# Kernel tuning notes

Measured on AMD Instinct MI355X. Metric: run time of the kernel, lower is better.

Reference implementation:

```python
import jax, jax.numpy as jnp
import numpy as np
from jax import lax

COEF = 0.97  # rnn.weight_hh_l0; weight_ih_l0 == 1.0


def setup_inputs() -> dict:
    key = jax.random.key(0)
    B, C, T = 128, 1, 262144
    x = jax.random.normal(key, (B, C, T), dtype=jnp.float32)
    return {"input": x}


def reference(input) -> jnp.ndarray:
    # torch.nn.RNN(1,1,1,bias=False) with weight_ih=1, weight_hh=COEF and
    # default nonlinearity='tanh':  h[t] = tanh(x[t] + COEF * h[t-1])
    x = input[:, 0, :]                     # [B, T]
    B = x.shape[0]

    def step(h, x_t):                      # h: [B], x_t: [B]
        h = jnp.tanh(x_t + COEF * h)
        return h, h

    h0 = jnp.zeros((B,), dtype=x.dtype)
    _, ys = lax.scan(step, h0, x.T)        # ys: [T, B]
    return ys.T[:, None, :]                # [B, 1, T]
```

## Files before the change

### kernel.cpp

```cpp
#include <hip/hip_runtime.h>


#define BB 128
#define TT 262144
#define LL 128
#define WW 64
#define KK 32
#define RR ((WW + LL) / KK)
#define WR (WW / KK)

typedef float f32x4 __attribute__((ext_vector_type(4)));

__global__ __launch_bounds__(256) void ipe_kernel(const float* __restrict__ x,
                                                  float* __restrict__ y) {
    const int tid  = threadIdx.x;
    const int lane = tid & 63;
    const int wv   = tid >> 6;
    const int w    = blockIdx.x * 4 + wv;
    const int wavesPerRow = (TT / LL) / 64;
    const int row  = w / wavesPerRow;
    const int qg   = w % wavesPerRow;
    const int s0   = qg * 64;
    const size_t rowBase = (size_t)row * TT;

    __shared__ float tile_all[4][64][36];
    float (*tile)[36] = tile_all[wv];

    const int ls = lane & 7;
    const int le = lane >> 3;
    const long loadBase = (long)(s0 + ls) * LL - WW + 4 * le;

    f32x4 pfA[8], pfB[8];

    auto issue = [&](f32x4 (&pf)[8], int r) {
        #pragma unroll
        for (int m = 0; m < 8; ++m) {
            const long t = loadBase + (long)m * 8 * LL + (long)r * KK;
            if (t >= 0) pf[m] = *reinterpret_cast<const f32x4*>(x + rowBase + t);
            else        pf[m] = (f32x4){0.f, 0.f, 0.f, 0.f};
        }
    };

    const float C2 = 2.885390081777926815f;
    const float K2 = 0.97f * C2;
    float h = 0.f;

    issue(pfA, 0);

    auto round = [&](f32x4 (&cur)[8], f32x4 (&nxt)[8], int r) {
        if (r + 1 < RR) issue(nxt, r + 1);

        #pragma unroll
        for (int m = 0; m < 8; ++m)
            *reinterpret_cast<f32x4*>(&tile[8 * m + ls][4 * le]) = cur[m];
        asm volatile("" ::: "memory");

        float xv[KK];
        #pragma unroll
        for (int e = 0; e < 8; ++e) {
            f32x4 v = *reinterpret_cast<const f32x4*>(&tile[lane][4 * e]);
            xv[4 * e + 0] = v.x; xv[4 * e + 1] = v.y;
            xv[4 * e + 2] = v.z; xv[4 * e + 3] = v.w;
        }

        #pragma unroll
        for (int k = 0; k < KK; ++k) {
            float z2 = fmaf(K2, h, xv[k] * C2);
            float ez = __builtin_amdgcn_exp2f(z2);
            float rc = __builtin_amdgcn_rcpf(ez + 1.0f);
            h = fmaf(-2.0f, rc, 1.0f);
            xv[k] = h;
        }

        if (r >= WR) {
            asm volatile("" ::: "memory");
            #pragma unroll
            for (int e = 0; e < 8; ++e) {
                f32x4 v;
                v.x = xv[4 * e + 0]; v.y = xv[4 * e + 1];
                v.z = xv[4 * e + 2]; v.w = xv[4 * e + 3];
                *reinterpret_cast<f32x4*>(&tile[lane][4 * e]) = v;
            }
            asm volatile("" ::: "memory");
            #pragma unroll
            for (int m = 0; m < 8; ++m) {
                f32x4 v = *reinterpret_cast<const f32x4*>(&tile[8 * m + ls][4 * le]);
                const long t = loadBase + (long)m * 8 * LL + (long)r * KK;
                __builtin_nontemporal_store(v, reinterpret_cast<f32x4*>(y + rowBase + t));
            }
        }
        asm volatile("" ::: "memory");
    };

    #pragma unroll 1
    for (int r = 0; r < RR; r += 2) {
        round(pfA, pfB, r);
        round(pfB, pfA, r + 1);
    }
}

extern "C" void kernel_launch(void* const* d_in, const int* in_sizes, int n_in,
                              void* d_out, int out_size, void* d_ws, size_t ws_size,
                              hipStream_t stream) {
    const float* x = (const float*)d_in[0];
    float* y = (float*)d_out;
    const int blocks = (BB * (TT / LL)) / (4 * 64);
    ipe_kernel<<<dim3(blocks), dim3(256), 0, stream>>>(x, y);
}
```

Measured before the change: 56.75 us.

## Use single-wave blocks with 64-step chunks, one-shot load, and swizzled LDS

Each 64-lane block now handles 64 consecutive chunks of 64 timesteps. It loads the whole span plus a 64-element warm-up window in one shot, replacing the double-buffered 32-step rounds of 128-step segments. The LDS tile uses an XOR swizzle instead of padding to avoid bank conflicts. Block IDs are remapped across XCDs, and the stores change from nontemporal to regular. The warm-up-to-output ratio rises from 1:2 to 1:1, which adds transcendental work in exchange for more parallelism and no loop or prefetch overhead. Holding 64 floats of state per lane raises register pressure.

New measurement: 46.84 us. 17.5% less time.

```diff
diff --git a/kernel.cpp b/kernel.cpp
--- a/kernel.cpp
+++ b/kernel.cpp
@@ -3,99 +3,102 @@
 
 #define BB 128
 #define TT 262144
-#define LL 128
-#define WW 64
-#define KK 32
-#define RR ((WW + LL) / KK)
-#define WR (WW / KK)
+#define CH 64
+#define SPW 64
+#define NBLK (BB * (TT / CH) / SPW)
 
 typedef float f32x4 __attribute__((ext_vector_type(4)));
 
-__global__ __launch_bounds__(256) void ipe_kernel(const float* __restrict__ x,
-                                                  float* __restrict__ y) {
-    const int tid  = threadIdx.x;
-    const int lane = tid & 63;
-    const int wv   = tid >> 6;
-    const int w    = blockIdx.x * 4 + wv;
-    const int wavesPerRow = (TT / LL) / 64;
-    const int row  = w / wavesPerRow;
-    const int qg   = w % wavesPerRow;
-    const int s0   = qg * 64;
+__global__ __launch_bounds__(64) void ipe_kernel(const float* __restrict__ x,
+                                                 float* __restrict__ y) {
+    const int lane = threadIdx.x;
+    const int bid = (blockIdx.x & 7) * (NBLK >> 3) + (blockIdx.x >> 3);
+    const int row = bid >> 6;
+    const int g   = bid & 63;
     const size_t rowBase = (size_t)row * TT;
+    const long   tileT0  = (long)g * (SPW * CH) - CH;
 
-    __shared__ float tile_all[4][64][36];
-    float (*tile)[36] = tile_all[wv];
+    __shared__ float tile[65 * 64];
 
-    const int ls = lane & 7;
-    const int le = lane >> 3;
-    const long loadBase = (long)(s0 + ls) * LL - WW + 4 * le;
+    const int h4 = lane >> 4;
+    const int t4 = lane & 15;
 
-    f32x4 pfA[8], pfB[8];
+    f32x4 pf[17];
+    #pragma unroll
+    for (int m = 0; m < 16; ++m) {
+        const long T = tileT0 + (long)(m * 64 + lane) * 4;
+        if (T >= 0) pf[m] = *reinterpret_cast<const f32x4*>(x + rowBase + T);
+        else        pf[m] = (f32x4){0.f, 0.f, 0.f, 0.f};
+    }
+    if (lane < 16) {
+        const long T = tileT0 + (long)(16 * 64 + lane) * 4;
+        pf[16] = *reinterpret_cast<const f32x4*>(x + rowBase + T);
+    }
 
-    auto issue = [&](f32x4 (&pf)[8], int r) {
-        #pragma unroll
-        for (int m = 0; m < 8; ++m) {
-            const long t = loadBase + (long)m * 8 * LL + (long)r * KK;
-            if (t >= 0) pf[m] = *reinterpret_cast<const f32x4*>(x + rowBase + t);
-            else        pf[m] = (f32x4){0.f, 0.f, 0.f, 0.f};
-        }
-    };
+    #pragma unroll
+    for (int m = 0; m < 16; ++m) {
+        const int span = 4 * m + h4;
+        *reinterpret_cast<f32x4*>(&tile[span * 64 + 4 * (t4 ^ (span & 15))]) = pf[m];
+    }
+    if (lane < 16) {
+        *reinterpret_cast<f32x4*>(&tile[64 * 64 + 4 * lane]) = pf[16];
+    }
+    asm volatile("" ::: "memory");
 
     const float C2 = 2.885390081777926815f;
     const float K2 = 0.97f * C2;
     float h = 0.f;
+    float xv[64];
 
-    issue(pfA, 0);
+    #pragma unroll
+    for (int e = 0; e < 16; ++e) {
+        f32x4 v = *reinterpret_cast<const f32x4*>(
+            &tile[lane * 64 + 4 * (e ^ (lane & 15))]);
+        xv[4 * e + 0] = v.x; xv[4 * e + 1] = v.y;
+        xv[4 * e + 2] = v.z; xv[4 * e + 3] = v.w;
+    }
+    #pragma unroll
+    for (int k = 0; k < 64; ++k) {
+        float z2 = fmaf(K2, h, xv[k] * C2);
+        float ez = __builtin_amdgcn_exp2f(z2);
+        float rc = __builtin_amdgcn_rcpf(ez + 1.0f);
+        h = fmaf(-2.0f, rc, 1.0f);
+    }
 
-    auto round = [&](f32x4 (&cur)[8], f32x4 (&nxt)[8], int r) {
-        if (r + 1 < RR) issue(nxt, r + 1);
+    const int sp1 = lane + 1;
+    #pragma unroll
+    for (int e = 0; e < 16; ++e) {
+        f32x4 v = *reinterpret_cast<const f32x4*>(
+            &tile[sp1 * 64 + 4 * (e ^ (sp1 & 15))]);
+        xv[4 * e + 0] = v.x; xv[4 * e + 1] = v.y;
+        xv[4 * e + 2] = v.z; xv[4 * e + 3] = v.w;
+    }
+    #pragma unroll
+    for (int k = 0; k < 64; ++k) {
+        float z2 = fmaf(K2, h, xv[k] * C2);
+        float ez = __builtin_amdgcn_exp2f(z2);
+        float rc = __builtin_amdgcn_rcpf(ez + 1.0f);
+        h = fmaf(-2.0f, rc, 1.0f);
+        xv[k] = h;
+    }
 
-        #pragma unroll
-        for (int m = 0; m < 8; ++m)
-            *reinterpret_cast<f32x4*>(&tile[8 * m + ls][4 * le]) = cur[m];
-        asm volatile("" ::: "memory");
+    asm volatile("" ::: "memory");
+    #pragma unroll
+    for (int e = 0; e < 16; ++e) {
+        f32x4 v;
+        v.x = xv[4 * e + 0]; v.y = xv[4 * e + 1];
+        v.z = xv[4 * e + 2]; v.w = xv[4 * e + 3];
+        *reinterpret_cast<f32x4*>(&tile[sp1 * 64 + 4 * (e ^ (sp1 & 15))]) = v;
+    }
+    asm volatile("" ::: "memory");
 
-        float xv[KK];
-        #pragma unroll
-        for (int e = 0; e < 8; ++e) {
-            f32x4 v = *reinterpret_cast<const f32x4*>(&tile[lane][4 * e]);
-            xv[4 * e + 0] = v.x; xv[4 * e + 1] = v.y;
-            xv[4 * e + 2] = v.z; xv[4 * e + 3] = v.w;
-        }
-
-        #pragma unroll
-        for (int k = 0; k < KK; ++k) {
-            float z2 = fmaf(K2, h, xv[k] * C2);
-            float ez = __builtin_amdgcn_exp2f(z2);
-            float rc = __builtin_amdgcn_rcpf(ez + 1.0f);
-            h = fmaf(-2.0f, rc, 1.0f);
-            xv[k] = h;
-        }
-
-        if (r >= WR) {
-            asm volatile("" ::: "memory");
-            #pragma unroll
-            for (int e = 0; e < 8; ++e) {
-                f32x4 v;
-                v.x = xv[4 * e + 0]; v.y = xv[4 * e + 1];
-                v.z = xv[4 * e + 2]; v.w = xv[4 * e + 3];
-                *reinterpret_cast<f32x4*>(&tile[lane][4 * e]) = v;
-            }
-            asm volatile("" ::: "memory");
-            #pragma unroll
-            for (int m = 0; m < 8; ++m) {
-                f32x4 v = *reinterpret_cast<const f32x4*>(&tile[8 * m + ls][4 * le]);
-                const long t = loadBase + (long)m * 8 * LL + (long)r * KK;
-                __builtin_nontemporal_store(v, reinterpret_cast<f32x4*>(y + rowBase + t));
-            }
-        }
-        asm volatile("" ::: "memory");
-    };
-
-    #pragma unroll 1
-    for (int r = 0; r < RR; r += 2) {
-        round(pfA, pfB, r);
-        round(pfB, pfA, r + 1);
+    const long outT0 = tileT0 + CH;
+    #pragma unroll
+    for (int m = 0; m < 16; ++m) {
+        const int span = 1 + 4 * m + h4;
+        f32x4 v = *reinterpret_cast<const f32x4*>(
+            &tile[span * 64 + 4 * (t4 ^ (span & 15))]);
+        *reinterpret_cast<f32x4*>(y + rowBase + outT0 + (long)(m * 64 + lane) * 4) = v;
     }
 }
 
@@ -104,6 +107,5 @@
                               hipStream_t stream) {
     const float* x = (const float*)d_in[0];
     float* y = (float*)d_out;
-    const int blocks = (BB * (TT / LL)) / (4 * 64);
-    ipe_kernel<<<dim3(blocks), dim3(256), 0, stream>>>(x, y);
+    ipe_kernel<<<dim3(NBLK), dim3(64), 0, stream>>>(x, y);
 }
```
